# Kernel optimization log

Hardware: AMD Instinct MI355X
Metric: run time of the kernel (lower is better)

The kernel has to match this reference:

```python
import jax, jax.numpy as jnp
import numpy as np

B, S, H, A, I = 64, 512, 1024, 1024, 1024


def setup_inputs() -> dict:
    key = jax.random.key(0)
    ks = jax.random.split(key, 12)
    s = lambda fan_in: 1.0 / np.sqrt(fan_in)
    return {
        "encoded": jax.random.normal(ks[0], (B, S, H), jnp.float32),
        "inputs": jax.random.normal(ks[1], (B, I), jnp.float32),
        "states": jax.random.normal(ks[2], (B, H), jnp.float32),
        # attention params
        "W_enc": jax.random.uniform(ks[3], (H, A), jnp.float32, -s(H), s(H)),
        "b_enc": jnp.zeros((A,), jnp.float32),
        "W_dec": jax.random.uniform(ks[4], (H, A), jnp.float32, -s(H), s(H)),
        "b_dec": jnp.zeros((A,), jnp.float32),
        "w_out": jax.random.uniform(ks[5], (A, 1), jnp.float32, -s(A), s(A)),
        "b_out": jnp.zeros((1,), jnp.float32),
        # GRU cell params (input size = I + H)
        "W_ih": jax.random.uniform(ks[6], (3 * H, I + H), jnp.float32, -s(H), s(H)),
        "W_hh": jax.random.uniform(ks[7], (3 * H, H), jnp.float32, -s(H), s(H)),
        "b_ih": jax.random.uniform(ks[8], (3 * H,), jnp.float32, -s(H), s(H)),
        "b_hh": jax.random.uniform(ks[9], (3 * H,), jnp.float32, -s(H), s(H)),
    }


def reference(encoded, inputs, states, W_enc, b_enc, W_dec, b_dec, w_out, b_out,
              W_ih, W_hh, b_ih, b_hh):
    # setup_memory: project encoder states  [B,S,H] @ [H,A] -> [B,S,A]
    enc_proj = jnp.einsum("bsh,ha->bsa", encoded, W_enc) + b_enc
    # project decoder state and broadcast over S
    dec_proj = states @ W_dec + b_dec                      # [B,A]
    projected = enc_proj + dec_proj[:, None, :]            # [B,S,A]
    scores = jnp.tanh(projected) @ w_out + b_out           # [B,S,1]
    weights = jax.nn.softmax(scores, axis=1)               # [B,S,1]
    attention = jnp.sum(encoded * weights, axis=1)         # [B,H]
    # GRU cell on concatenated input
    x = jnp.concatenate([inputs, attention], axis=1)       # [B,I+H]
    gi = x @ W_ih.T + b_ih                                 # [B,3H]
    gh = states @ W_hh.T + b_hh                            # [B,3H]
    i_r, i_z, i_n = jnp.split(gi, 3, axis=1)
    h_r, h_z, h_n = jnp.split(gh, 3, axis=1)
    r = jax.nn.sigmoid(i_r + h_r)
    z = jax.nn.sigmoid(i_z + h_z)
    n = jnp.tanh(i_n + r * h_n)
    return (1.0 - z) * n + z * states                      # [B,H]
```

## Files before the change

kernel.cpp:

```cpp
#include <hip/hip_runtime.h>
#include <stdint.h>

typedef __bf16 bf16x8 __attribute__((ext_vector_type(8)));
typedef float f32x4 __attribute__((ext_vector_type(4)));

#define LOG2E 1.4426950408889634f
#define LSTR 32

__device__ __forceinline__ unsigned short f2bf(float f) {
  unsigned int x = __builtin_bit_cast(unsigned int, f);
  x += 0x7FFFu + ((x >> 16) & 1u);
  return (unsigned short)(x >> 16);
}
__device__ __forceinline__ float bflo(unsigned int u) {
  return __builtin_bit_cast(float, u << 16);
}
__device__ __forceinline__ float bfhi(unsigned int u) {
  return __builtin_bit_cast(float, u & 0xffff0000u);
}
__device__ __forceinline__ float tanh_fast(float x) {
  float cx = fminf(fmaxf(x, -15.f), 15.f);
  float e = __builtin_amdgcn_exp2f(cx * (2.f * LOG2E));
  return (e - 1.f) * __builtin_amdgcn_rcpf(e + 1.f);
}
__device__ __forceinline__ float sigmoid_fast(float x) {
  float cx = fminf(fmaxf(x, -30.f), 30.f);
  float e = __builtin_amdgcn_exp2f(cx * LOG2E);
  return e * __builtin_amdgcn_rcpf(e + 1.f);
}
__device__ __forceinline__ ushort4 cvt4(const float4 f) {
  return make_ushort4(f2bf(f.x), f2bf(f.y), f2bf(f.z), f2bf(f.w));
}

__device__ __forceinline__ void gl_lds16(const unsigned short* g,
                                         const unsigned short* lds_base) {
  __builtin_amdgcn_global_load_lds(
      (const __attribute__((address_space(1))) unsigned int*)(uintptr_t)g,
      (__attribute__((address_space(3))) unsigned int*)(unsigned int)(uintptr_t)lds_base,
      16, 0, 0);
}

__global__ __launch_bounds__(256) void k_prep(
    const float* __restrict__ W_enc, unsigned short* __restrict__ Wt,
    const float* __restrict__ states, const float* __restrict__ W_dec,
    const float* __restrict__ b_dec, const float* __restrict__ b_enc,
    float* __restrict__ dvec, float4* __restrict__ zbase,
    const float* __restrict__ enc, unsigned short* __restrict__ encb) {
  __shared__ unsigned short tile[64][65];
  __shared__ float red[256];
  const int bid = blockIdx.x;
  const int tid = threadIdx.x;
  if (bid < 256) {
    const int bx = bid & 15, by = bid >> 4;
    const int x = tid & 63, y0 = tid >> 6;
#pragma unroll
    for (int i = y0; i < 64; i += 4)
      tile[i][x] = f2bf(W_enc[(size_t)(by * 64 + i) * 1024 + bx * 64 + x]);
    __syncthreads();
#pragma unroll
    for (int i = y0; i < 64; i += 4)
      Wt[(size_t)(bx * 64 + i) * 1024 + by * 64 + x] = tile[x][i];
  } else if (bid < 768) {
    const int bb = bid - 256;
    const int b = bb >> 3;
    const int a0 = (bb & 7) * 128;
    const int a = tid & 127, half = tid >> 7;
    const float* sp = states + (size_t)b * 1024;
    const float* wp = W_dec + a0 + a;
    float acc = 0.f;
    const int kb = half * 512;
#pragma unroll 8
    for (int k = kb; k < kb + 512; ++k)
      acc += sp[k] * wp[(size_t)k * 1024];
    red[tid] = acc;
    __syncthreads();
    if (tid < 128) {
      float v = red[tid] + red[tid + 128];
      dvec[(size_t)b * 1024 + a0 + tid] = v + b_dec[a0 + tid] + b_enc[a0 + tid];
    }
  } else if (bid < 800) {
    const float4 z = {0.f, 0.f, 0.f, 0.f};
    zbase[(size_t)(bid - 768) * 256 + tid] = z;
  } else {
    const size_t i = ((size_t)(bid - 800) * 256 + tid) * 8;
    const float4 f0 = *(const float4*)(enc + i);
    const float4 f1 = *(const float4*)(enc + i + 4);
    *(ushort4*)(encb + i) = cvt4(f0);
    *(ushort4*)(encb + i + 4) = cvt4(f1);
  }
}

__global__ __launch_bounds__(256, 3) void k_scores_bf16(
    const unsigned short* __restrict__ encb,
    const unsigned short* __restrict__ Wt,
    const float* __restrict__ dvec,
    const float* __restrict__ w_out,
    float* __restrict__ scores) {
  __shared__ alignas(16) unsigned short lds[2][8192];
  __shared__ float sc[128];

  const int tid = threadIdx.x;
  const int wave = tid >> 6, lane = tid & 63;
  const int l15 = lane & 15, quad = lane >> 4;
  const int xcd = blockIdx.x & 7;
  const int kb_ = blockIdx.x >> 3;
  const int mt = ((kb_ >> 3) << 3) | xcd;
  const int nt = kb_ & 7;
  const int row0 = mt * 128;
  const int b = row0 >> 9;
  const int wm = (wave >> 1) * 64, wn = (wave & 1) * 64;
  const int srow = lane >> 2;
  const int fsw = ((lane >> 2) & 3) ^ ((lane >> 4) & 3);
  const int skoff = (((lane & 3) ^ fsw) * 8);
  const int rchunk = ((quad ^ ((l15 & 3) ^ ((l15 >> 2) & 3))) * 8);

  if (tid < 128) sc[tid] = 0.f;

  const unsigned short* gsrc[4];
#pragma unroll
  for (int s = 0; s < 4; ++s) {
    const int g = wave * 4 + s;
    gsrc[s] = (g < 8)
        ? encb + (size_t)(row0 + g * 16 + srow) * 1024 + skoff
        : Wt + (size_t)(nt * 128 + (g - 8) * 16 + srow) * 1024 + skoff;
  }

  const f32x4 vz = {0.f, 0.f, 0.f, 0.f};
  f32x4 acc[4][4];
#pragma unroll
  for (int i = 0; i < 4; ++i)
#pragma unroll
    for (int j = 0; j < 4; ++j) acc[i][j] = vz;

#define STAGE(BUF, KK)                                              \
  do {                                                              \
    _Pragma("unroll") for (int s = 0; s < 4; ++s)                   \
        gl_lds16(gsrc[s] + (KK), &lds[BUF][(wave * 4 + s) * 512]);  \
  } while (0)

#define COMPUTE(BUF)                                                          \
  do {                                                                        \
    bf16x8 af[4], bg[4];                                                      \
    _Pragma("unroll") for (int i = 0; i < 4; ++i)                             \
        af[i] = *(const bf16x8*)(&lds[BUF][(wm + i * 16 + l15) * LSTR + rchunk]); \
    _Pragma("unroll") for (int j = 0; j < 4; ++j)                             \
        bg[j] = *(const bf16x8*)(&lds[BUF][4096 + (wn + j * 16 + l15) * LSTR + rchunk]); \
    _Pragma("unroll") for (int i = 0; i < 4; ++i)                             \
      _Pragma("unroll") for (int j = 0; j < 4; ++j)                           \
          acc[i][j] = __builtin_amdgcn_mfma_f32_16x16x32_bf16(af[i], bg[j],   \
                                                              acc[i][j], 0, 0, 0); \
  } while (0)

  STAGE(0, 0);
  __syncthreads();

#pragma unroll 1
  for (int k0 = 0; k0 < 1024; k0 += 64) {
    STAGE(1, k0 + 32);
    COMPUTE(0);
    __syncthreads();
    if (k0 + 64 < 1024) { STAGE(0, k0 + 64); }
    COMPUTE(1);
    __syncthreads();
  }
#undef STAGE
#undef COMPUTE

  float p[4][4];
#pragma unroll
  for (int i = 0; i < 4; ++i)
#pragma unroll
    for (int r = 0; r < 4; ++r) p[i][r] = 0.f;
#pragma unroll
  for (int j = 0; j < 4; ++j) {
    const int a = nt * 128 + wn + j * 16 + l15;
    const float dv = dvec[(size_t)b * 1024 + a];
    const float wo = w_out[a];
#pragma unroll
    for (int i = 0; i < 4; ++i)
#pragma unroll
      for (int r = 0; r < 4; ++r)
        p[i][r] += tanh_fast(acc[i][j][r] + dv) * wo;
  }
#pragma unroll
  for (int i = 0; i < 4; ++i)
#pragma unroll
    for (int r = 0; r < 4; ++r) {
      float v = p[i][r];
      v += __shfl_xor(v, 1);
      v += __shfl_xor(v, 2);
      v += __shfl_xor(v, 4);
      v += __shfl_xor(v, 8);
      if (l15 == 0) atomicAdd(&sc[wm + i * 16 + quad * 4 + r], v);
    }
  __syncthreads();
  if (tid < 128)
    atomicAdd(&scores[(size_t)b * 512 + (row0 & 511) + tid], sc[tid]);
}

__global__ __launch_bounds__(256) void k_scores_f32(
    const float* __restrict__ enc, const unsigned short* __restrict__ Wt,
    const float* __restrict__ dvec, const float* __restrict__ w_out,
    float* __restrict__ scores) {
  __shared__ alignas(16) unsigned short lA[128 * LSTR];
  __shared__ alignas(16) unsigned short lB[128 * LSTR];
  __shared__ float sc[128];
  const int tid = threadIdx.x;
  const int wave = tid >> 6, lane = tid & 63;
  const int l15 = lane & 15, quad = lane >> 4;
  const int mt = blockIdx.x >> 2, nh = blockIdx.x & 3;
  const int row0 = mt * 128, b = row0 >> 9;
  const int wm = (wave >> 1) * 64, wn = (wave & 1) * 64;
  const int srow = lane >> 2, skoff = (lane & 3) * 8;
  if (tid < 128) sc[tid] = 0.f;
  const f32x4 vz = {0.f, 0.f, 0.f, 0.f};
#pragma unroll 1
  for (int t2 = 0; t2 < 2; ++t2) {
    const int nt = nh * 2 + t2;
    f32x4 acc[4][4];
#pragma unroll
    for (int i = 0; i < 4; ++i)
#pragma unroll
      for (int j = 0; j < 4; ++j) acc[i][j] = vz;
#pragma unroll 1
    for (int k0 = 0; k0 < 1024; k0 += 32) {
      ushort4 sa[2][2];
      uint4 vb[2];
#pragma unroll
      for (int rr = 0; rr < 2; ++rr) {
        const int r = wave * 2 + rr;
        const float* ap = enc + (size_t)(row0 + r * 16 + srow) * 1024 + k0 + skoff;
        sa[rr][0] = cvt4(*(const float4*)ap);
        sa[rr][1] = cvt4(*(const float4*)(ap + 4));
        vb[rr] = *(const uint4*)(Wt + (size_t)(nt * 128 + r * 16 + srow) * 1024 + k0 + skoff);
      }
      __syncthreads();
#pragma unroll
      for (int rr = 0; rr < 2; ++rr) {
        const int r = wave * 2 + rr;
        *(ushort4*)(lA + (r * 16 + srow) * LSTR + skoff) = sa[rr][0];
        *(ushort4*)(lA + (r * 16 + srow) * LSTR + skoff + 4) = sa[rr][1];
        *(uint4*)(lB + (r * 16 + srow) * LSTR + skoff) = vb[rr];
      }
      __syncthreads();
      bf16x8 af[4], bg[4];
#pragma unroll
      for (int i = 0; i < 4; ++i)
        af[i] = *(const bf16x8*)(lA + (wm + i * 16 + l15) * LSTR + quad * 8);
#pragma unroll
      for (int j = 0; j < 4; ++j)
        bg[j] = *(const bf16x8*)(lB + (wn + j * 16 + l15) * LSTR + quad * 8);
#pragma unroll
      for (int i = 0; i < 4; ++i)
#pragma unroll
        for (int j = 0; j < 4; ++j)
          acc[i][j] = __builtin_amdgcn_mfma_f32_16x16x32_bf16(af[i], bg[j],
                                                              acc[i][j], 0, 0, 0);
    }
    float p[4][4];
#pragma unroll
    for (int i = 0; i < 4; ++i)
#pragma unroll
      for (int r = 0; r < 4; ++r) p[i][r] = 0.f;
#pragma unroll
    for (int j = 0; j < 4; ++j) {
      const int a = nt * 128 + wn + j * 16 + l15;
      const float dv = dvec[(size_t)b * 1024 + a];
      const float wo = w_out[a];
#pragma unroll
      for (int i = 0; i < 4; ++i)
#pragma unroll
        for (int r = 0; r < 4; ++r)
          p[i][r] += tanh_fast(acc[i][j][r] + dv) * wo;
    }
#pragma unroll
    for (int i = 0; i < 4; ++i)
#pragma unroll
      for (int r = 0; r < 4; ++r) {
        float v = p[i][r];
        v += __shfl_xor(v, 1);
        v += __shfl_xor(v, 2);
        v += __shfl_xor(v, 4);
        v += __shfl_xor(v, 8);
        if (l15 == 0) atomicAdd(&sc[wm + i * 16 + quad * 4 + r], v);
      }
  }
  __syncthreads();
  if (tid < 128)
    atomicAdd(&scores[(size_t)b * 512 + (row0 & 511) + tid], sc[tid]);
}

template <bool ABF16>
__global__ __launch_bounds__(256) void k_attn(const void* __restrict__ encv,
                                              const float* __restrict__ scores,
                                              float* __restrict__ att2) {
  const int b = blockIdx.x >> 4;
  const int hch = (blockIdx.x >> 1) & 7;
  const int sh = blockIdx.x & 1;
  const int tid = threadIdx.x;
  __shared__ float w[512];
  __shared__ float redm[4], reds[4];
  __shared__ float red[16][132];

  const float s0 = scores[(size_t)b * 512 + tid];
  const float s1 = scores[(size_t)b * 512 + 256 + tid];
  float m = fmaxf(s0, s1);
#pragma unroll
  for (int off = 32; off; off >>= 1) m = fmaxf(m, __shfl_xor(m, off));
  const int wv = tid >> 6;
  if ((tid & 63) == 0) redm[wv] = m;
  __syncthreads();
  m = fmaxf(fmaxf(redm[0], redm[1]), fmaxf(redm[2], redm[3]));
  const float e0 = __builtin_amdgcn_exp2f((s0 - m) * LOG2E);
  const float e1 = __builtin_amdgcn_exp2f((s1 - m) * LOG2E);
  float sum = e0 + e1;
#pragma unroll
  for (int off = 32; off; off >>= 1) sum += __shfl_xor(sum, off);
  if ((tid & 63) == 0) reds[wv] = sum;
  __syncthreads();
  sum = reds[0] + reds[1] + reds[2] + reds[3];
  const float inv = 1.f / sum;
  w[tid] = e0 * inv;
  w[tid + 256] = e1 * inv;
  __syncthreads();

  const int sgrp = tid >> 4;
  const int hsub = tid & 15;
  const int h0 = hch * 128 + hsub * 8;
  float a[8];
#pragma unroll
  for (int j = 0; j < 8; ++j) a[j] = 0.f;
#pragma unroll 8
  for (int si = 0; si < 16; ++si) {
    const int s = sh * 256 + si * 16 + sgrp;
    const float ws_ = w[s];
    if constexpr (ABF16) {
      const uint4 v = *(const uint4*)((const unsigned short*)encv +
                                      (size_t)(b * 512 + s) * 1024 + h0);
      a[0] += ws_ * bflo(v.x); a[1] += ws_ * bfhi(v.x);
      a[2] += ws_ * bflo(v.y); a[3] += ws_ * bfhi(v.y);
      a[4] += ws_ * bflo(v.z); a[5] += ws_ * bfhi(v.z);
      a[6] += ws_ * bflo(v.w); a[7] += ws_ * bfhi(v.w);
    } else {
      const float* ep = (const float*)encv + (size_t)(b * 512 + s) * 1024 + h0;
      const float4 v0 = *(const float4*)ep;
      const float4 v1 = *(const float4*)(ep + 4);
      a[0] += ws_ * v0.x; a[1] += ws_ * v0.y;
      a[2] += ws_ * v0.z; a[3] += ws_ * v0.w;
      a[4] += ws_ * v1.x; a[5] += ws_ * v1.y;
      a[6] += ws_ * v1.z; a[7] += ws_ * v1.w;
    }
  }
#pragma unroll
  for (int j = 0; j < 8; ++j) red[sgrp][hsub * 8 + j] = a[j];
  __syncthreads();
#pragma unroll
  for (int step = 8; step >= 1; step >>= 1) {
    if (sgrp < step) {
#pragma unroll
      for (int j = 0; j < 8; ++j)
        red[sgrp][hsub * 8 + j] += red[sgrp + step][hsub * 8 + j];
    }
    __syncthreads();
  }
  if (sgrp == 0) {
    float* op = att2 + ((size_t)sh * 64 + b) * 1024 + h0;
    float4 o0 = {red[0][hsub * 8 + 0], red[0][hsub * 8 + 1],
                 red[0][hsub * 8 + 2], red[0][hsub * 8 + 3]};
    float4 o1 = {red[0][hsub * 8 + 4], red[0][hsub * 8 + 5],
                 red[0][hsub * 8 + 6], red[0][hsub * 8 + 7]};
    *(float4*)op = o0;
    *(float4*)(op + 4) = o1;
  }
}

__global__ __launch_bounds__(256) void k_gru_gemm(
    const float* __restrict__ xin,
    const float* __restrict__ att2,
    const float* __restrict__ states,
    const float* __restrict__ W_ih,
    const float* __restrict__ W_hh,
    float* __restrict__ gbuf) {
  const int tid = threadIdx.x;
  const int wave = tid >> 6, lane = tid & 63;
  const int l15 = lane & 15, quad = lane >> 4;
  const int kk = blockIdx.x & 7;
  const int rest = blockIdx.x >> 3;
  const bool is_gh = rest >= 48;
  const int nt = is_gh ? rest - 48 : rest;
  const int n0 = nt * 64;
  const int KT = is_gh ? 1024 : 2048;
  const int Kh = KT >> 3;
  const int kbase = kk * Kh;
  const float* W = is_gh ? W_hh : W_ih;
  const int plane = is_gh ? 8 + kk : kk;
  float* outp = gbuf + (size_t)plane * 64 * 3072;

  __shared__ alignas(16) unsigned short lA[64 * LSTR];
  __shared__ alignas(16) unsigned short lB[64 * LSTR];

  const f32x4 vz = {0.f, 0.f, 0.f, 0.f};
  f32x4 acc[2][2];
  acc[0][0] = vz; acc[0][1] = vz; acc[1][0] = vz; acc[1][1] = vz;

  const int arow = tid >> 2;
  const int achunk = (tid & 3) * 8;
  const int fswG = ((tid >> 2) & 3) ^ ((tid >> 4) & 3);
  const int wchunk = (((tid & 3) ^ fswG) * 8);
  const int rchunkG = ((quad ^ ((l15 & 3) ^ ((l15 >> 2) & 3))) * 8);
  const int wm2 = (wave >> 1) * 32, wn2 = (wave & 1) * 32;

  float4 ra0, ra1, rb0, rb1;
  auto LOADK = [&](int kg0) {
    const int kg = kg0 + achunk;
    if (is_gh) {
      const float* ap = states + (size_t)arow * 1024 + kg;
      ra0 = *(const float4*)ap;
      ra1 = *(const float4*)(ap + 4);
    } else if (kg < 1024) {
      const float* ap = xin + (size_t)arow * 1024 + kg;
      ra0 = *(const float4*)ap;
      ra1 = *(const float4*)(ap + 4);
    } else {
      const float* p0 = att2 + (size_t)arow * 1024 + (kg - 1024);
      const float* p1 = p0 + (size_t)64 * 1024;
      const float4 x0 = *(const float4*)p0, y0 = *(const float4*)p1;
      const float4 x1 = *(const float4*)(p0 + 4), y1 = *(const float4*)(p1 + 4);
      ra0 = make_float4(x0.x + y0.x, x0.y + y0.y, x0.z + y0.z, x0.w + y0.w);
      ra1 = make_float4(x1.x + y1.x, x1.y + y1.y, x1.z + y1.z, x1.w + y1.w);
    }
    const float* wp = W + (size_t)(n0 + arow) * KT + kg;
    rb0 = *(const float4*)wp;
    rb1 = *(const float4*)(wp + 4);
  };
  LOADK(kbase);

#pragma unroll 1
  for (int k0 = 0; k0 < Kh; k0 += 32) {
    __syncthreads();
    *(ushort4*)(lA + arow * LSTR + wchunk) = cvt4(ra0);
    *(ushort4*)(lA + arow * LSTR + wchunk + 4) = cvt4(ra1);
    *(ushort4*)(lB + arow * LSTR + wchunk) = cvt4(rb0);
    *(ushort4*)(lB + arow * LSTR + wchunk + 4) = cvt4(rb1);
    __syncthreads();
    if (k0 + 32 < Kh) LOADK(kbase + k0 + 32);
    bf16x8 af[2], bg[2];
#pragma unroll
    for (int i = 0; i < 2; ++i)
      af[i] = *(const bf16x8*)(lA + (wm2 + i * 16 + l15) * LSTR + rchunkG);
#pragma unroll
    for (int j = 0; j < 2; ++j)
      bg[j] = *(const bf16x8*)(lB + (wn2 + j * 16 + l15) * LSTR + rchunkG);
#pragma unroll
    for (int i = 0; i < 2; ++i)
#pragma unroll
      for (int j = 0; j < 2; ++j)
        acc[i][j] = __builtin_amdgcn_mfma_f32_16x16x32_bf16(af[i], bg[j],
                                                            acc[i][j], 0, 0, 0);
  }
#pragma unroll
  for (int i = 0; i < 2; ++i)
#pragma unroll
    for (int j = 0; j < 2; ++j)
#pragma unroll
      for (int r = 0; r < 4; ++r) {
        const int m = wm2 + i * 16 + quad * 4 + r;
        const int n = n0 + wn2 + j * 16 + l15;
        outp[(size_t)m * 3072 + n] = acc[i][j][r];
      }
}

__global__ void k_gate(const float* __restrict__ gbuf,
                       const float* __restrict__ states,
                       const float* __restrict__ b_ih,
                       const float* __restrict__ b_hh,
                       float* __restrict__ outp) {
  const int idx = blockIdx.x * 256 + threadIdx.x;
  const int b = idx >> 10, h = idx & 1023;
  float gir = 0.f, giz = 0.f, gin = 0.f, ghr = 0.f, ghz = 0.f, ghn = 0.f;
#pragma unroll
  for (int p = 0; p < 8; ++p) {
    const float* gi = gbuf + ((size_t)p * 64 + b) * 3072;
    gir += gi[h]; giz += gi[1024 + h]; gin += gi[2048 + h];
    const float* gh = gbuf + ((size_t)(8 + p) * 64 + b) * 3072;
    ghr += gh[h]; ghz += gh[1024 + h]; ghn += gh[2048 + h];
  }
  const float ir = gir + b_ih[h];
  const float iz = giz + b_ih[1024 + h];
  const float in_ = gin + b_ih[2048 + h];
  const float hr = ghr + b_hh[h];
  const float hz = ghz + b_hh[1024 + h];
  const float hn = ghn + b_hh[2048 + h];
  const float r = sigmoid_fast(ir + hr);
  const float z = sigmoid_fast(iz + hz);
  const float n = tanh_fast(in_ + r * hn);
  const float hp = states[idx];
  outp[idx] = (1.f - z) * n + z * hp;
}

extern "C" void kernel_launch(void* const* d_in, const int* in_sizes, int n_in,
                              void* d_out, int out_size, void* d_ws, size_t ws_size,
                              hipStream_t stream) {
  const float* enc    = (const float*)d_in[0];
  const float* xin    = (const float*)d_in[1];
  const float* states = (const float*)d_in[2];
  const float* W_enc  = (const float*)d_in[3];
  const float* b_enc  = (const float*)d_in[4];
  const float* W_dec  = (const float*)d_in[5];
  const float* b_dec  = (const float*)d_in[6];
  const float* w_out  = (const float*)d_in[7];
  const float* W_ih   = (const float*)d_in[9];
  const float* W_hh   = (const float*)d_in[10];
  const float* b_ih   = (const float*)d_in[11];
  const float* b_hh   = (const float*)d_in[12];
  float* out = (float*)d_out;

  const size_t ENC_BF16_BYTES = (size_t)32768 * 1024 * 2;
  const bool use_bf16 = ws_size >= ENC_BF16_BYTES + (8u << 20);

  char* ws = (char*)d_ws;
  unsigned short* encb = (unsigned short*)ws;
  char* base = ws + (use_bf16 ? ENC_BF16_BYTES : 0);
  unsigned short* Wt = (unsigned short*)base;
  float* dvec    = (float*)(base + 2097152);
  float* scoresb = (float*)(base + 2097152 + 262144);
  float* att2    = (float*)(base + 2097152 + 262144 + 131072);
  float* gbuf = use_bf16 ? (float*)ws : (float*)(base + (4u << 20));

  const int prep_grid = use_bf16 ? 17184 : 800;
  k_prep<<<prep_grid, 256, 0, stream>>>(W_enc, Wt, states, W_dec, b_dec, b_enc,
                                        dvec, (float4*)scoresb, enc, encb);
  if (use_bf16) {
    k_scores_bf16<<<2048, 256, 0, stream>>>(encb, Wt, dvec, w_out, scoresb);
    k_attn<true><<<1024, 256, 0, stream>>>(encb, scoresb, att2);
  } else {
    k_scores_f32<<<1024, 256, 0, stream>>>(enc, Wt, dvec, w_out, scoresb);
    k_attn<false><<<1024, 256, 0, stream>>>(enc, scoresb, att2);
  }
  k_gru_gemm<<<768, 256, 0, stream>>>(xin, att2, states, W_ih, W_hh, gbuf);
  k_gate<<<256, 256, 0, stream>>>(gbuf, states, b_ih, b_hh, out);
}
```

Baseline: 393.1 us.

## Fuse fp32-to-bf16 encoder conversion into the scores GEMM kernel

The separate prep pass that converted the whole encoder tensor to bf16 is removed. The scores GEMM now stages fp32 encoder tiles straight into LDS, converts them to bf16 in registers, and has one set of waves (nt==0) write the bf16 copy out for the attention kernel. The goal is to avoid one full fp32 read plus bf16 write pass over the encoder. In exchange, each of the eight N-tiles now reads fp32 A tiles, doubling A-side global traffic and LDS footprint (48KB per buffer pair), which may reduce occupancy.

Result: slower. 437.8 us (+11.4%).

```diff
diff --git a/kernel.cpp b/kernel.cpp
--- a/kernel.cpp
+++ b/kernel.cpp
@@ -31,9 +31,16 @@
 __device__ __forceinline__ ushort4 cvt4(const float4 f) {
   return make_ushort4(f2bf(f.x), f2bf(f.y), f2bf(f.z), f2bf(f.w));
 }
-
-__device__ __forceinline__ void gl_lds16(const unsigned short* g,
-                                         const unsigned short* lds_base) {
+__device__ __forceinline__ bf16x8 cvt8c(const f32x4 lo, const f32x4 hi) {
+  bf16x8 r;
+  r[0] = (__bf16)lo[0]; r[1] = (__bf16)lo[1];
+  r[2] = (__bf16)lo[2]; r[3] = (__bf16)lo[3];
+  r[4] = (__bf16)hi[0]; r[5] = (__bf16)hi[1];
+  r[6] = (__bf16)hi[2]; r[7] = (__bf16)hi[3];
+  return r;
+}
+
+__device__ __forceinline__ void gl_lds16(const void* g, const void* lds_base) {
   __builtin_amdgcn_global_load_lds(
       (const __attribute__((address_space(1))) unsigned int*)(uintptr_t)g,
       (__attribute__((address_space(3))) unsigned int*)(unsigned int)(uintptr_t)lds_base,
@@ -44,8 +51,7 @@
     const float* __restrict__ W_enc, unsigned short* __restrict__ Wt,
     const float* __restrict__ states, const float* __restrict__ W_dec,
     const float* __restrict__ b_dec, const float* __restrict__ b_enc,
-    float* __restrict__ dvec, float4* __restrict__ zbase,
-    const float* __restrict__ enc, unsigned short* __restrict__ encb) {
+    float* __restrict__ dvec, float4* __restrict__ zbase) {
   __shared__ unsigned short tile[64][65];
   __shared__ float red[256];
   const int bid = blockIdx.x;
@@ -78,25 +84,20 @@
       float v = red[tid] + red[tid + 128];
       dvec[(size_t)b * 1024 + a0 + tid] = v + b_dec[a0 + tid] + b_enc[a0 + tid];
     }
-  } else if (bid < 800) {
+  } else {
     const float4 z = {0.f, 0.f, 0.f, 0.f};
     zbase[(size_t)(bid - 768) * 256 + tid] = z;
-  } else {
-    const size_t i = ((size_t)(bid - 800) * 256 + tid) * 8;
-    const float4 f0 = *(const float4*)(enc + i);
-    const float4 f1 = *(const float4*)(enc + i + 4);
-    *(ushort4*)(encb + i) = cvt4(f0);
-    *(ushort4*)(encb + i + 4) = cvt4(f1);
-  }
-}
-
-__global__ __launch_bounds__(256, 3) void k_scores_bf16(
-    const unsigned short* __restrict__ encb,
+  }
+}
+
+__global__ __launch_bounds__(256, 3) void k_scoresF(
+    const float* __restrict__ enc,
     const unsigned short* __restrict__ Wt,
     const float* __restrict__ dvec,
     const float* __restrict__ w_out,
-    float* __restrict__ scores) {
-  __shared__ alignas(16) unsigned short lds[2][8192];
+    float* __restrict__ scores,
+    unsigned short* __restrict__ encb) {
+  __shared__ alignas(16) unsigned char lds[2][24576];
   __shared__ float sc[128];
 
   const int tid = threadIdx.x;
@@ -109,21 +110,30 @@
   const int row0 = mt * 128;
   const int b = row0 >> 9;
   const int wm = (wave >> 1) * 64, wn = (wave & 1) * 64;
+  const bool sidew = (nt == 0) && ((wave & 1) == 0);
+
+  const int arow_lo = lane >> 3;
+  const int csw = (lane & 7) ^ arow_lo;
+  const float* srcA[4];
+#pragma unroll
+  for (int s = 0; s < 4; ++s) {
+    const int g = wave * 4 + s;
+    srcA[s] = enc + (size_t)(row0 + g * 8 + arow_lo) * 1024 + csw * 4;
+  }
   const int srow = lane >> 2;
   const int fsw = ((lane >> 2) & 3) ^ ((lane >> 4) & 3);
   const int skoff = (((lane & 3) ^ fsw) * 8);
+  const unsigned short* srcB[2];
+#pragma unroll
+  for (int s = 0; s < 2; ++s) {
+    const int reg = wave * 2 + s;
+    srcB[s] = Wt + (size_t)(nt * 128 + reg * 16 + srow) * 1024 + skoff;
+  }
   const int rchunk = ((quad ^ ((l15 & 3) ^ ((l15 >> 2) & 3))) * 8);
+  const int aslot0 = ((quad << 1) ^ (l15 & 7)) << 4;
+  const int aslot1 = aslot0 ^ 16;
 
   if (tid < 128) sc[tid] = 0.f;
-
-  const unsigned short* gsrc[4];
-#pragma unroll
-  for (int s = 0; s < 4; ++s) {
-    const int g = wave * 4 + s;
-    gsrc[s] = (g < 8)
-        ? encb + (size_t)(row0 + g * 16 + srow) * 1024 + skoff
-        : Wt + (size_t)(nt * 128 + (g - 8) * 16 + srow) * 1024 + skoff;
-  }
 
   const f32x4 vz = {0.f, 0.f, 0.f, 0.f};
   f32x4 acc[4][4];
@@ -132,24 +142,44 @@
 #pragma unroll
     for (int j = 0; j < 4; ++j) acc[i][j] = vz;
 
-#define STAGE(BUF, KK)                                              \
-  do {                                                              \
-    _Pragma("unroll") for (int s = 0; s < 4; ++s)                   \
-        gl_lds16(gsrc[s] + (KK), &lds[BUF][(wave * 4 + s) * 512]);  \
-  } while (0)
-
-#define COMPUTE(BUF)                                                          \
-  do {                                                                        \
-    bf16x8 af[4], bg[4];                                                      \
-    _Pragma("unroll") for (int i = 0; i < 4; ++i)                             \
-        af[i] = *(const bf16x8*)(&lds[BUF][(wm + i * 16 + l15) * LSTR + rchunk]); \
-    _Pragma("unroll") for (int j = 0; j < 4; ++j)                             \
-        bg[j] = *(const bf16x8*)(&lds[BUF][4096 + (wn + j * 16 + l15) * LSTR + rchunk]); \
-    _Pragma("unroll") for (int i = 0; i < 4; ++i)                             \
-      _Pragma("unroll") for (int j = 0; j < 4; ++j)                           \
-          acc[i][j] = __builtin_amdgcn_mfma_f32_16x16x32_bf16(af[i], bg[j],   \
-                                                              acc[i][j], 0, 0, 0); \
-  } while (0)
+  auto STAGE = [&](int bi, int kk) {
+    unsigned char* Ab = &lds[bi][0];
+    unsigned char* Bb = &lds[bi][16384];
+#pragma unroll
+    for (int s = 0; s < 4; ++s)
+      gl_lds16(srcA[s] + kk, Ab + (wave * 4 + s) * 1024);
+#pragma unroll
+    for (int s = 0; s < 2; ++s)
+      gl_lds16(srcB[s] + kk, Bb + (wave * 2 + s) * 1024);
+  };
+  auto COMPUTE = [&](int bi, int kcur) {
+    const unsigned char* Ab = &lds[bi][0];
+    const unsigned short* Bb = (const unsigned short*)&lds[bi][16384];
+    bf16x8 af[4], bg[4];
+#pragma unroll
+    for (int i = 0; i < 4; ++i) {
+      const unsigned char* ap = Ab + ((wm + i * 16 + l15) << 7);
+      const f32x4 lo = *(const f32x4*)(ap + aslot0);
+      const f32x4 hi = *(const f32x4*)(ap + aslot1);
+      af[i] = cvt8c(lo, hi);
+    }
+    if (sidew) {
+#pragma unroll
+      for (int i = 0; i < 4; ++i) {
+        const int row = row0 + wm + i * 16 + l15;
+        *(bf16x8*)(encb + (size_t)row * 1024 + kcur + quad * 8) = af[i];
+      }
+    }
+#pragma unroll
+    for (int j = 0; j < 4; ++j)
+      bg[j] = *(const bf16x8*)(Bb + (wn + j * 16 + l15) * LSTR + rchunk);
+#pragma unroll
+    for (int i = 0; i < 4; ++i)
+#pragma unroll
+      for (int j = 0; j < 4; ++j)
+        acc[i][j] = __builtin_amdgcn_mfma_f32_16x16x32_bf16(af[i], bg[j],
+                                                            acc[i][j], 0, 0, 0);
+  };
 
   STAGE(0, 0);
   __syncthreads();
@@ -157,14 +187,12 @@
 #pragma unroll 1
   for (int k0 = 0; k0 < 1024; k0 += 64) {
     STAGE(1, k0 + 32);
-    COMPUTE(0);
+    COMPUTE(0, k0);
     __syncthreads();
     if (k0 + 64 < 1024) { STAGE(0, k0 + 64); }
-    COMPUTE(1);
-    __syncthreads();
-  }
-#undef STAGE
-#undef COMPUTE
+    COMPUTE(1, k0 + 32);
+    __syncthreads();
+  }
 
   float p[4][4];
 #pragma unroll
@@ -527,11 +555,10 @@
   float* att2    = (float*)(base + 2097152 + 262144 + 131072);
   float* gbuf = use_bf16 ? (float*)ws : (float*)(base + (4u << 20));
 
-  const int prep_grid = use_bf16 ? 17184 : 800;
-  k_prep<<<prep_grid, 256, 0, stream>>>(W_enc, Wt, states, W_dec, b_dec, b_enc,
-                                        dvec, (float4*)scoresb, enc, encb);
+  k_prep<<<800, 256, 0, stream>>>(W_enc, Wt, states, W_dec, b_dec, b_enc,
+                                  dvec, (float4*)scoresb);
   if (use_bf16) {
-    k_scores_bf16<<<2048, 256, 0, stream>>>(encb, Wt, dvec, w_out, scoresb);
+    k_scoresF<<<2048, 256, 0, stream>>>(enc, Wt, dvec, w_out, scoresb, encb);
     k_attn<true><<<1024, 256, 0, stream>>>(encb, scoresb, att2);
   } else {
     k_scores_f32<<<1024, 256, 0, stream>>>(enc, Wt, dvec, w_out, scoresb);
```
